# Performance work log

Measured on AMD Instinct MI355X. Metric: run time of the kernel, lower is better.

## Reference

```python
import jax, jax.numpy as jnp
import numpy as np

T, B = 1024, 16384

def setup_inputs() -> dict:
    key = jax.random.key(0)
    ks = jax.random.split(key, 8)
    return {
        "inputs": jax.random.normal(ks[0], (T, B, 6), dtype=jnp.float32),
        "targets": jax.random.normal(ks[1], (T, B, 1), dtype=jnp.float32),
        "Wx": jax.random.normal(ks[2], (6, 6), dtype=jnp.float32) * 0.3,
        "Wu": jax.random.normal(ks[3], (6, 1), dtype=jnp.float32) * 0.3,
        "W1": jax.random.normal(ks[4], (20, 12), dtype=jnp.float32) * 0.3,
        "b1": jax.random.normal(ks[5], (20,), dtype=jnp.float32) * 0.1,
        "W2": jax.random.normal(ks[6], (1, 20), dtype=jnp.float32) * 0.3,
        "b2": jax.random.normal(ks[7], (1,), dtype=jnp.float32) * 0.1,
        "epoch": 10,
        "maxepoch": 100,
        "forceswitch": 2,
    }

def reference(inputs, targets, Wx, Wu, W1, b1, W2, b2, epoch, maxepoch, forceswitch):
    # forceswitch == 2 => deterministic teacher forcing: the feedback `output`
    # at step k is targets[k-1] for k > 0 and zeros at k = 0.
    assert forceswitch == 2
    Tlen, Bsz, _ = inputs.shape
    prev_out = jnp.concatenate(
        [jnp.zeros((1, Bsz, 1), dtype=inputs.dtype), targets[:-1]], axis=0
    )  # [T, B, 1]

    def step(db, xs):
        x_k, u_k = xs  # [B, 6], [B, 1]
        db = db @ Wx.T + u_k @ Wu.T                 # delay buffer update [B, 6]
        ni = jnp.concatenate([db, x_k], axis=-1)    # [B, 12]
        h = jnp.tanh(ni @ W1.T + b1)                # [B, 20]
        out = h @ W2.T + b2                         # [B, 1]
        return db, out

    db0 = jnp.zeros((Bsz, 6), dtype=inputs.dtype)
    _, outputs = jax.lax.scan(step, db0, (inputs, prev_out))
    return outputs  # [T, B, 1]
```

## Files before the change

kernel.cpp:

```cpp
#include <hip/hip_runtime.h>
#include <cstddef>

#define TT 1024
#define BB 16384
#define LC 32
#define CC (TT / LC)

__device__ __forceinline__ float pade_tanh(float x) {
    float cx = fminf(fmaxf(x, -4.97f), 4.97f);
    float s  = cx * cx;
    float n  = cx * fmaf(s, fmaf(s, (s + 378.0f), 17325.0f), 135135.0f);
    float d  = fmaf(s, fmaf(s, fmaf(s, 28.0f, 3150.0f), 62370.0f), 135135.0f);
    return n * __builtin_amdgcn_rcpf(d);
}

__global__ __launch_bounds__(256) void k_phase1(
    const float* __restrict__ targets,
    const float* __restrict__ Wx,
    const float* __restrict__ Wu,
    float* __restrict__ v)
{
    const int b = blockIdx.x * 256 + threadIdx.x;
    const int c = blockIdx.y;
    float wx[6][6], wu[6];
#pragma unroll
    for (int i = 0; i < 6; ++i) {
        wu[i] = Wu[i];
#pragma unroll
        for (int j = 0; j < 6; ++j) wx[i][j] = Wx[i * 6 + j];
    }
    float db[6] = {0.f, 0.f, 0.f, 0.f, 0.f, 0.f};
    const int t0 = c * LC;
#pragma unroll 4
    for (int s = 0; s < LC; ++s) {
        const int t = t0 + s;
        float u = 0.0f;
        if (t > 0) u = targets[(size_t)(t - 1) * BB + b];
        float nd[6];
#pragma unroll
        for (int i = 0; i < 6; ++i) {
            float a = u * wu[i];
#pragma unroll
            for (int j = 0; j < 6; ++j) a = fmaf(db[j], wx[i][j], a);
            nd[i] = a;
        }
#pragma unroll
        for (int i = 0; i < 6; ++i) db[i] = nd[i];
    }
#pragma unroll
    for (int i = 0; i < 6; ++i) v[((size_t)c * 6 + i) * BB + b] = db[i];
}

__global__ __launch_bounds__(256) void k_phase2(
    const float* __restrict__ Wx,
    float* __restrict__ v)
{
    const int b = blockIdx.x * 256 + threadIdx.x;
    float M[6][6];
#pragma unroll
    for (int i = 0; i < 6; ++i)
#pragma unroll
        for (int j = 0; j < 6; ++j)
            M[j][i] = Wx[i * 6 + j];
    for (int it = 0; it < 5; ++it) {
        float P[6][6];
#pragma unroll
        for (int i = 0; i < 6; ++i)
#pragma unroll
            for (int j = 0; j < 6; ++j) {
                float a = 0.0f;
#pragma unroll
                for (int k = 0; k < 6; ++k) a = fmaf(M[i][k], M[k][j], a);
                P[i][j] = a;
            }
#pragma unroll
        for (int i = 0; i < 6; ++i)
#pragma unroll
            for (int j = 0; j < 6; ++j) M[i][j] = P[i][j];
    }
    float db[6] = {0.f, 0.f, 0.f, 0.f, 0.f, 0.f};
    for (int c = 0; c < CC; ++c) {
        float vv[6];
#pragma unroll
        for (int i = 0; i < 6; ++i) {
            const size_t idx = ((size_t)c * 6 + i) * BB + b;
            vv[i] = v[idx];
            v[idx] = db[i];
        }
        float nd[6];
#pragma unroll
        for (int i = 0; i < 6; ++i) {
            float a = vv[i];
#pragma unroll
            for (int j = 0; j < 6; ++j) a = fmaf(db[j], M[j][i], a);
            nd[i] = a;
        }
#pragma unroll
        for (int i = 0; i < 6; ++i) db[i] = nd[i];
    }
}

__global__ __launch_bounds__(256, 2) void k_phase3(
    const float* __restrict__ inputs,
    const float* __restrict__ targets,
    const float* __restrict__ Wxg,
    const float* __restrict__ Wug,
    const float* __restrict__ W1g,
    const float* __restrict__ b1g,
    const float* __restrict__ W2g,
    const float* __restrict__ b2g,
    const float* __restrict__ dbs,
    float* __restrict__ out)
{
    const int tid  = threadIdx.x;
    const int half = tid & 1;
    const int b    = blockIdx.x * 128 + (tid >> 1);
    const int c    = blockIdx.y;
    const int m0   = half * 10;

    float wx[6][6], wu[6];
#pragma unroll
    for (int i = 0; i < 6; ++i) {
        wu[i] = Wug[i];
#pragma unroll
        for (int j = 0; j < 6; ++j) wx[i][j] = Wxg[i * 6 + j];
    }
    const float vb2 = b2g[0];

    float2 w1p[5][12];
    float2 vb1[5], vw2[5];
#pragma unroll
    for (int p = 0; p < 5; ++p) {
        const int ma = m0 + p, mb = m0 + p + 5;
#pragma unroll
        for (int j = 0; j < 12; ++j) {
            w1p[p][j].x = W1g[ma * 12 + j];
            w1p[p][j].y = W1g[mb * 12 + j];
        }
        vb1[p].x = b1g[ma]; vb1[p].y = b1g[mb];
        vw2[p].x = W2g[ma]; vw2[p].y = W2g[mb];
    }

    float db[6];
#pragma unroll
    for (int i = 0; i < 6; ++i) db[i] = dbs[((size_t)c * 6 + i) * BB + b];

    const int t0 = c * LC;
    float u_cur = (t0 == 0) ? 0.0f : targets[(size_t)(t0 - 1) * BB + b];
    const float2* xp = reinterpret_cast<const float2*>(inputs + ((size_t)t0 * BB + b) * 6);
    float2 x0 = xp[0], x1 = xp[1], x2 = xp[2];

    for (int s = 0; s < LC; ++s) {
        const int t = t0 + s;
        float u_nxt = 0.0f;
        float2 n0 = x0, n1 = x1, n2 = x2;
        if (s + 1 < LC) {
            u_nxt = targets[(size_t)t * BB + b];
            const float2* xpn =
                reinterpret_cast<const float2*>(inputs + ((size_t)(t + 1) * BB + b) * 6);
            n0 = xpn[0]; n1 = xpn[1]; n2 = xpn[2];
        }

        float nd[6];
#pragma unroll
        for (int i = 0; i < 6; ++i) {
            float a = u_cur * wu[i];
#pragma unroll
            for (int j = 0; j < 6; ++j) a = fmaf(db[j], wx[i][j], a);
            nd[i] = a;
        }
#pragma unroll
        for (int i = 0; i < 6; ++i) db[i] = nd[i];

        const float ni[12] = {db[0], db[1], db[2], db[3], db[4], db[5],
                              x0.x, x0.y, x1.x, x1.y, x2.x, x2.y};

        float2 acc[5];
#pragma unroll
        for (int p = 0; p < 5; ++p) acc[p] = vb1[p];
#pragma unroll
        for (int j = 0; j < 12; ++j) {
            const float nij = ni[j];
#pragma unroll
            for (int p = 0; p < 5; ++p) {
                acc[p].x = fmaf(w1p[p][j].x, nij, acc[p].x);
                acc[p].y = fmaf(w1p[p][j].y, nij, acc[p].y);
            }
        }

        float2 osum = {0.0f, 0.0f};
#pragma unroll
        for (int p = 0; p < 5; ++p) {
            float tx = pade_tanh(acc[p].x);
            float ty = pade_tanh(acc[p].y);
            osum.x = fmaf(vw2[p].x, tx, osum.x);
            osum.y = fmaf(vw2[p].y, ty, osum.y);
        }
        float oh = osum.x + osum.y;
        float o  = oh + __shfl_xor(oh, 1, 64) + vb2;
        if (half == 0) out[(size_t)t * BB + b] = o;

        u_cur = u_nxt; x0 = n0; x1 = n1; x2 = n2;
    }
}

extern "C" void kernel_launch(void* const* d_in, const int* in_sizes, int n_in,
                              void* d_out, int out_size, void* d_ws, size_t ws_size,
                              hipStream_t stream) {
    (void)in_sizes; (void)n_in; (void)out_size; (void)ws_size;
    const float* inputs  = (const float*)d_in[0];
    const float* targets = (const float*)d_in[1];
    const float* Wx = (const float*)d_in[2];
    const float* Wu = (const float*)d_in[3];
    const float* W1 = (const float*)d_in[4];
    const float* b1 = (const float*)d_in[5];
    const float* W2 = (const float*)d_in[6];
    const float* b2 = (const float*)d_in[7];
    float* out = (float*)d_out;
    float* v   = (float*)d_ws;

    dim3 blk(256);
    dim3 g1(BB / 256, CC);
    hipLaunchKernelGGL(k_phase1, g1, blk, 0, stream, targets, Wx, Wu, v);
    hipLaunchKernelGGL(k_phase2, dim3(BB / 256), blk, 0, stream, Wx, v);
    dim3 g3(BB / 128, CC);
    hipLaunchKernelGGL(k_phase3, g3, blk, 0, stream,
                       inputs, targets, Wx, Wu, W1, b1, W2, b2, v, out);
}
```

Measured before the change: 818.1 us.

## Split hidden units across four lanes per batch element with packed FMA and exp-based tanh

The phase-3 kernel now gives each batch element to four threads with five hidden units each, instead of two threads with ten. Block coverage drops from 128 to 64 elements and the grid doubles. The hidden layer uses packed two-wide vector FMAs and a two-step shuffle reduction. The Pade tanh is replaced with an exp2-plus-reciprocal form, and pointer striding replaces index arithmetic. This cuts per-thread serial work and raises the occupancy target, at the cost of redundantly recomputing the 6x6 delay-buffer recurrence in four lanes and more duplicated input loads.

```diff
diff --git a/kernel.cpp b/kernel.cpp
--- a/kernel.cpp
+++ b/kernel.cpp
@@ -6,12 +6,11 @@
 #define LC 32
 #define CC (TT / LC)
 
-__device__ __forceinline__ float pade_tanh(float x) {
-    float cx = fminf(fmaxf(x, -4.97f), 4.97f);
-    float s  = cx * cx;
-    float n  = cx * fmaf(s, fmaf(s, (s + 378.0f), 17325.0f), 135135.0f);
-    float d  = fmaf(s, fmaf(s, fmaf(s, 28.0f, 3150.0f), 62370.0f), 135135.0f);
-    return n * __builtin_amdgcn_rcpf(d);
+typedef float v2f __attribute__((ext_vector_type(2)));
+
+__device__ __forceinline__ float fast_tanh(float x) {
+    float e = exp2f(x * 2.8853900817779268f);
+    return fmaf(-2.0f, __builtin_amdgcn_rcpf(e + 1.0f), 1.0f);
 }
 
 __global__ __launch_bounds__(256) void k_phase1(
@@ -100,7 +99,7 @@
     }
 }
 
-__global__ __launch_bounds__(256, 2) void k_phase3(
+__global__ __launch_bounds__(256, 4) void k_phase3(
     const float* __restrict__ inputs,
     const float* __restrict__ targets,
     const float* __restrict__ Wxg,
@@ -112,11 +111,11 @@
     const float* __restrict__ dbs,
     float* __restrict__ out)
 {
-    const int tid  = threadIdx.x;
-    const int half = tid & 1;
-    const int b    = blockIdx.x * 128 + (tid >> 1);
-    const int c    = blockIdx.y;
-    const int m0   = half * 10;
+    const int tid = threadIdx.x;
+    const int q   = tid & 3;
+    const int b   = blockIdx.x * 64 + (tid >> 2);
+    const int c   = blockIdx.y;
+    const int m0  = q * 5;
 
     float wx[6][6], wu[6];
 #pragma unroll
@@ -127,38 +126,44 @@
     }
     const float vb2 = b2g[0];
 
-    float2 w1p[5][12];
-    float2 vb1[5], vw2[5];
-#pragma unroll
-    for (int p = 0; p < 5; ++p) {
-        const int ma = m0 + p, mb = m0 + p + 5;
-#pragma unroll
-        for (int j = 0; j < 12; ++j) {
-            w1p[p][j].x = W1g[ma * 12 + j];
-            w1p[p][j].y = W1g[mb * 12 + j];
-        }
-        vb1[p].x = b1g[ma]; vb1[p].y = b1g[mb];
-        vw2[p].x = W2g[ma]; vw2[p].y = W2g[mb];
-    }
+    v2f w01[12], w23[12];
+    float w4[12];
+#pragma unroll
+    for (int j = 0; j < 12; ++j) {
+        w01[j] = (v2f){W1g[(m0 + 0) * 12 + j], W1g[(m0 + 1) * 12 + j]};
+        w23[j] = (v2f){W1g[(m0 + 2) * 12 + j], W1g[(m0 + 3) * 12 + j]};
+        w4[j]  = W1g[(m0 + 4) * 12 + j];
+    }
+    const v2f b01 = (v2f){b1g[m0 + 0], b1g[m0 + 1]};
+    const v2f b23 = (v2f){b1g[m0 + 2], b1g[m0 + 3]};
+    const float b4 = b1g[m0 + 4];
+    const v2f wo01 = (v2f){W2g[m0 + 0], W2g[m0 + 1]};
+    const v2f wo23 = (v2f){W2g[m0 + 2], W2g[m0 + 3]};
+    const float wo4 = W2g[m0 + 4];
 
     float db[6];
 #pragma unroll
     for (int i = 0; i < 6; ++i) db[i] = dbs[((size_t)c * 6 + i) * BB + b];
 
     const int t0 = c * LC;
-    float u_cur = (t0 == 0) ? 0.0f : targets[(size_t)(t0 - 1) * BB + b];
-    const float2* xp = reinterpret_cast<const float2*>(inputs + ((size_t)t0 * BB + b) * 6);
-    float2 x0 = xp[0], x1 = xp[1], x2 = xp[2];
+    const float* xptr = inputs + ((size_t)t0 * BB + b) * 6;
+    const float* tptr = targets + (size_t)t0 * BB + b;
+    float* optr = out + (size_t)t0 * BB + b;
+
+    float u_cur = (t0 == 0) ? 0.0f : tptr[-(ptrdiff_t)BB];
+    v2f x0 = *(const v2f*)(xptr);
+    v2f x1 = *(const v2f*)(xptr + 2);
+    v2f x2 = *(const v2f*)(xptr + 4);
 
     for (int s = 0; s < LC; ++s) {
-        const int t = t0 + s;
         float u_nxt = 0.0f;
-        float2 n0 = x0, n1 = x1, n2 = x2;
+        v2f n0 = x0, n1 = x1, n2 = x2;
         if (s + 1 < LC) {
-            u_nxt = targets[(size_t)t * BB + b];
-            const float2* xpn =
-                reinterpret_cast<const float2*>(inputs + ((size_t)(t + 1) * BB + b) * 6);
-            n0 = xpn[0]; n1 = xpn[1]; n2 = xpn[2];
+            u_nxt = *tptr;
+            const float* xn = xptr + (size_t)BB * 6;
+            n0 = *(const v2f*)(xn);
+            n1 = *(const v2f*)(xn + 2);
+            n2 = *(const v2f*)(xn + 4);
         }
 
         float nd[6];
@@ -175,32 +180,35 @@
         const float ni[12] = {db[0], db[1], db[2], db[3], db[4], db[5],
                               x0.x, x0.y, x1.x, x1.y, x2.x, x2.y};
 
-        float2 acc[5];
-#pragma unroll
-        for (int p = 0; p < 5; ++p) acc[p] = vb1[p];
+        v2f a01 = b01, a23 = b23;
+        float a4 = b4;
 #pragma unroll
         for (int j = 0; j < 12; ++j) {
-            const float nij = ni[j];
-#pragma unroll
-            for (int p = 0; p < 5; ++p) {
-                acc[p].x = fmaf(w1p[p][j].x, nij, acc[p].x);
-                acc[p].y = fmaf(w1p[p][j].y, nij, acc[p].y);
-            }
-        }
-
-        float2 osum = {0.0f, 0.0f};
-#pragma unroll
-        for (int p = 0; p < 5; ++p) {
-            float tx = pade_tanh(acc[p].x);
-            float ty = pade_tanh(acc[p].y);
-            osum.x = fmaf(vw2[p].x, tx, osum.x);
-            osum.y = fmaf(vw2[p].y, ty, osum.y);
-        }
-        float oh = osum.x + osum.y;
-        float o  = oh + __shfl_xor(oh, 1, 64) + vb2;
-        if (half == 0) out[(size_t)t * BB + b] = o;
+            const v2f nj = (v2f){ni[j], ni[j]};
+            a01 = __builtin_elementwise_fma(w01[j], nj, a01);
+            a23 = __builtin_elementwise_fma(w23[j], nj, a23);
+            a4  = fmaf(w4[j], ni[j], a4);
+        }
+
+        float t0u = fast_tanh(a01.x);
+        float t1u = fast_tanh(a01.y);
+        float t2u = fast_tanh(a23.x);
+        float t3u = fast_tanh(a23.y);
+        float t4u = fast_tanh(a4);
+        float o = wo01.x * t0u;
+        o = fmaf(wo01.y, t1u, o);
+        o = fmaf(wo23.x, t2u, o);
+        o = fmaf(wo23.y, t3u, o);
+        o = fmaf(wo4,    t4u, o);
+
+        o += __shfl_xor(o, 1, 64);
+        o += __shfl_xor(o, 2, 64);
+        if (q == 0) *optr = o + vb2;
 
         u_cur = u_nxt; x0 = n0; x1 = n1; x2 = n2;
+        xptr += (size_t)BB * 6;
+        tptr += BB;
+        optr += BB;
     }
 }
 
@@ -223,7 +231,7 @@
     dim3 g1(BB / 256, CC);
     hipLaunchKernelGGL(k_phase1, g1, blk, 0, stream, targets, Wx, Wu, v);
     hipLaunchKernelGGL(k_phase2, dim3(BB / 256), blk, 0, stream, Wx, v);
-    dim3 g3(BB / 128, CC);
+    dim3 g3(BB / 64, CC);
     hipLaunchKernelGGL(k_phase3, g3, blk, 0, stream,
                        inputs, targets, Wx, Wu, W1, b1, W2, b2, v, out);
 }
```

Result: faster. 785.1 us (-4.0%).
